# Optimization experiments

Hardware: AMD Instinct MI355X
Metric: run time of the kernel (lower is better)

The kernel has to match this reference:

```python
import jax, jax.numpy as jnp
import numpy as np

# Clebsch-Gordan coefficients in the real basis; l=1 components stored in (y,z,x) order
S2 = 1.0 / np.sqrt(2.0)
S3 = 1.0 / np.sqrt(3.0)
S6 = 1.0 / np.sqrt(6.0)
_C2 = np.zeros((5, 3, 3), np.float32)
_C2[0, 2, 0] = _C2[0, 0, 2] = S2          # ~ xy
_C2[1, 0, 1] = _C2[1, 1, 0] = S2          # ~ yz
_C2[2, 1, 1] = 2.0 * S6                   # ~ 2z^2 - x^2 - y^2
_C2[2, 2, 2] = -S6
_C2[2, 0, 0] = -S6
_C2[3, 2, 1] = _C2[3, 1, 2] = S2          # ~ xz
_C2[4, 2, 2] = S2                          # ~ x^2 - y^2
_C2[4, 0, 0] = -S2
C2 = jnp.asarray(_C2)

N0, N1 = 64, 32        # multiplicities of input 0e / 1o irreps
CUTOFF = 5.0


def basis_functions(pos):
    """pos [N,3] -> (scalars [N,64], l=1 features [N,32,3])."""
    r = jnp.linalg.norm(pos, axis=-1, keepdims=True) + 1e-9        # [N,1]
    d = pos[:, (1, 2, 0)] / r                                       # unit dir, (y,z,x) order
    c0 = jnp.linspace(0.0, CUTOFF, N0, dtype=pos.dtype)
    c1 = jnp.linspace(0.0, CUTOFF, N1, dtype=pos.dtype)
    f0 = jnp.exp(-4.0 * (r - c0) ** 2)                              # [N,64] gaussian RBF
    f1 = jnp.exp(-4.0 * (r - c1) ** 2)                              # [N,32]
    x1 = f1[:, :, None] * d[:, None, :]                             # [N,32,3]
    return f0, x1


def lin_l(x, W):
    # channel mixing within one irrep block; preserves the m axis if present
    if x.ndim == 2:
        return x @ W
    return jnp.einsum('ncm,cd->ndm', x, W)


def tensor_product(a0, a1, b0, b1):
    """Full uvw CG tensor product of (64x0 + 32x1) x (64x0 + 32x1)."""
    N = a0.shape[0]
    # l=0 outputs: 0x0->0 and 1x1->0
    p000 = jnp.einsum('na,nb->nab', a0, b0).reshape(N, -1)                 # [N,4096]
    p110 = jnp.einsum('nam,nbm->nab', a1, b1).reshape(N, -1) * S3          # [N,1024]
    t0 = jnp.concatenate([p000, p110], axis=1)                             # [N,5120]
    # l=1 outputs: 0x1->1, 1x0->1, 1x1->1 (cross product)
    p011 = (a0[:, :, None, None] * b1[:, None, :, :]).reshape(N, -1, 3)    # [N,2048,3]
    p101 = (a1[:, :, None, :] * b0[:, None, :, None]).reshape(N, -1, 3)    # [N,2048,3]
    p111 = (jnp.cross(a1[:, :, None, :], b1[:, None, :, :]) * S2).reshape(N, -1, 3)
    t1 = jnp.concatenate([p011, p101, p111], axis=1)                       # [N,5120,3]
    # l=2 output: 1x1->2 via CG tensor
    t2 = jnp.einsum('nai,nbj,mij->nabm', a1, b1, C2).reshape(N, -1, 5)     # [N,1024,5]
    return t0, t1, t2


def setup_inputs() -> dict:
    key = jax.random.key(0)
    ks = jax.random.split(key, 10)
    N = 4096
    def w(k, i, o):
        return jax.random.normal(k, (i, o), jnp.float32) / np.sqrt(i)
    return {
        'positions': jax.random.normal(ks[0], (N, 3), jnp.float32) * 2.0,
        'W1_0': w(ks[1], 64, 64),
        'W1_1': w(ks[2], 32, 32),
        'W2_0': w(ks[3], 64, 64),
        'W2_1': w(ks[4], 32, 32),
        'W3_0': w(ks[5], 5120, 64),
        'W3_1': w(ks[6], 5120, 32),
        'W3_2': w(ks[7], 1024, 16),
        'W_out': w(ks[8], 240, 7),
        'b_out': jnp.zeros((7,), jnp.float32),
    }


def reference(positions, W1_0, W1_1, W2_0, W2_1, W3_0, W3_1, W3_2, W_out, b_out):
    f0, f1 = basis_functions(positions)                 # 64x0, 32x1
    a0, a1 = lin_l(f0, W1_0), lin_l(f1, W1_1)           # linear1
    b0, b1 = lin_l(f0, W2_0), lin_l(f1, W2_1)           # linear2
    t0, t1, t2 = tensor_product(a0, a1, b0, b1)         # 5120x0, 5120x1, 1024x2
    y0 = lin_l(t0, W3_0)                                # [N,64]
    y1 = lin_l(t1, W3_1)                                # [N,32,3]
    y2 = lin_l(t2, W3_2)                                # [N,16,5]
    N = y0.shape[0]
    feat = jnp.concatenate([y0, y1.reshape(N, -1), y2.reshape(N, -1)], axis=1)  # [N,240]
    return feat @ W_out + b_out                         # [N,7]
```

## Files before the change

### kernel.cpp

```cpp
#include <hip/hip_runtime.h>
#include <math.h>

#define NS2 0.70710678118654752440f
#define NS3 0.57735026918962576451f
#define NS6 0.40824829046386301636f

typedef _Float16 half8 __attribute__((ext_vector_type(8)));

#define OFF_W2   0
#define OFF_GRP  90112
#define GRP_STRIDE 5120

__global__ __launch_bounds__(256) void prep_kernel(
    const float* __restrict__ pos,
    const float* __restrict__ W1_0, const float* __restrict__ W1_1,
    const float* __restrict__ W2_0, const float* __restrict__ W2_1,
    const float* __restrict__ W3_0, const float* __restrict__ W3_1,
    const float* __restrict__ W3_2, const float* __restrict__ Wout,
    const float* __restrict__ bout,
    float* __restrict__ ws, float* __restrict__ out, int N)
{
    __shared__ float smem[2464];
    const int tid = threadIdx.x;

    if (blockIdx.x < 88) {
        float* s_wo = smem;
        for (int i = tid; i < 1680; i += 256) s_wo[i] = Wout[i];
        __syncthreads();
        int R = blockIdx.x * 256 + tid;
        int it = R >> 6, l = R & 63;
        float acc[7] = {0.f,0.f,0.f,0.f,0.f,0.f,0.f};
        if (it < 64) {
            const float* wr = W3_0 + (it*64 + l) * 64;
            #pragma unroll 4
            for (int o = 0; o < 64; o += 4) {
                float4 wv = *(const float4*)(wr + o);
                const float* w0 = s_wo + o * 7;
                #pragma unroll
                for (int k = 0; k < 7; ++k)
                    acc[k] = fmaf(wv.x, w0[k], fmaf(wv.y, w0[7+k],
                             fmaf(wv.z, w0[14+k], fmaf(wv.w, w0[21+k], acc[k]))));
            }
        } else if (it < 160) {
            int s = it - 64, m = s >> 5, a = s & 31;
            const float* wr = W3_1 + (2048 + a*64 + l) * 32;
            #pragma unroll 4
            for (int o = 0; o < 32; o += 4) {
                float4 wv = *(const float4*)(wr + o);
                const float* w0 = s_wo + (64 + o*3 + m) * 7;
                #pragma unroll
                for (int k = 0; k < 7; ++k)
                    acc[k] = fmaf(wv.x, w0[k], fmaf(wv.y, w0[21+k],
                             fmaf(wv.z, w0[42+k], fmaf(wv.w, w0[63+k], acc[k]))));
            }
        } else {
            int it2 = it - 160, ah = l >> 5, bh = l & 31;
            if (it2 < 16) {
                int a = it2*2 + ah;
                const float* wr = W3_0 + (4096 + a*32 + bh) * 64;
                #pragma unroll 4
                for (int o = 0; o < 64; o += 4) {
                    float4 wv = *(const float4*)(wr + o);
                    const float* w0 = s_wo + o * 7;
                    #pragma unroll
                    for (int k = 0; k < 7; ++k)
                        acc[k] = fmaf(wv.x, w0[k], fmaf(wv.y, w0[7+k],
                                 fmaf(wv.z, w0[14+k], fmaf(wv.w, w0[21+k], acc[k]))));
                }
            } else if (it2 < 112) {
                int u2 = it2 - 16, m = u2 >> 5, a = (u2 & 31)*2 + ah;
                const float* wr = W3_1 + (a*32 + bh) * 32;
                #pragma unroll 4
                for (int o = 0; o < 32; o += 4) {
                    float4 wv = *(const float4*)(wr + o);
                    const float* w0 = s_wo + (64 + o*3 + m) * 7;
                    #pragma unroll
                    for (int k = 0; k < 7; ++k)
                        acc[k] = fmaf(wv.x, w0[k], fmaf(wv.y, w0[21+k],
                                 fmaf(wv.z, w0[42+k], fmaf(wv.w, w0[63+k], acc[k]))));
                }
            } else {
                int u2 = it2 - 112, m = u2 >> 4, a = (u2 & 15)*2 + ah;
                const float* wr = W3_2 + (a*32 + bh) * 16;
                #pragma unroll 4
                for (int o = 0; o < 16; o += 4) {
                    float4 wv = *(const float4*)(wr + o);
                    const float* w0 = s_wo + (160 + o*5 + m) * 7;
                    #pragma unroll
                    for (int k = 0; k < 7; ++k)
                        acc[k] = fmaf(wv.x, w0[k], fmaf(wv.y, w0[35+k],
                                 fmaf(wv.z, w0[70+k], fmaf(wv.w, w0[105+k], acc[k]))));
                }
            }
        }
        half8 h;
        #pragma unroll
        for (int k = 0; k < 7; ++k) h[k] = (_Float16)acc[k];
        h[7] = (_Float16)0.f;
        *(half8*)((char*)ws + (size_t)R * 16) = h;
        return;
    }

    float* s_f0   = smem;
    float* s_f1   = smem + 512;
    float* s_a0   = smem + 768;
    float* s_b0   = smem + 1280;
    float* s_A1   = smem + 1792;
    float* s_B1   = smem + 2048;
    float* s_geom = smem + 2304;

    const int g    = blockIdx.x - 88;
    const int base = g * 8;
    float* grp = ws + OFF_GRP + (size_t)g * GRP_STRIDE;
    {
        int d = tid & 63;
        #pragma unroll
        for (int jj = 0; jj < 2; ++jj) {
            int j = (tid >> 6) + jj * 4;
            int n = base + j;
            float px = pos[n*3+0], py = pos[n*3+1], pz = pos[n*3+2];
            float r  = sqrtf(px*px + py*py + pz*pz) + 1e-9f;
            float t0 = r - (5.0f/63.0f) * (float)d;
            s_f0[j*64 + d] = __expf(-4.f * t0 * t0);
        }
        {
            int j = tid >> 5, d1 = tid & 31;
            int n = base + j;
            float px = pos[n*3+0], py = pos[n*3+1], pz = pos[n*3+2];
            float r  = sqrtf(px*px + py*py + pz*pz) + 1e-9f;
            float t1 = r - (5.0f/31.0f) * (float)d1;
            s_f1[j*32 + d1] = __expf(-4.f * t1 * t1);
        }
        if (tid < 8) {
            int n = base + tid;
            float px = pos[n*3+0], py = pos[n*3+1], pz = pos[n*3+2];
            float r  = sqrtf(px*px + py*py + pz*pz) + 1e-9f;
            float iv = 1.0f / r;
            float d0 = py*iv, d1 = pz*iv, d2 = px*iv;
            s_geom[0*8 + tid] = d0;
            s_geom[1*8 + tid] = d1;
            s_geom[2*8 + tid] = d2;
            s_geom[3*8 + tid] = NS3 * (d0*d0 + d1*d1 + d2*d2);
            s_geom[4*8 + tid] = 2.f*NS2*d2*d0;
            s_geom[5*8 + tid] = 2.f*NS2*d0*d1;
            s_geom[6*8 + tid] = NS6*(2.f*d1*d1 - d2*d2 - d0*d0);
            s_geom[7*8 + tid] = 2.f*NS2*d2*d1;
            s_geom[8*8 + tid] = NS2*(d2*d2 - d0*d0);
        }
        if (tid < 56) out[base*7 + tid] = bout[tid % 7];
    }
    __syncthreads();
    {
        int c = tid & 63, jb = tid >> 6;
        float aa0 = 0.f, aa1 = 0.f, ba0 = 0.f, ba1 = 0.f;
        const float* wa = W1_0 + c;
        const float* wb = W2_0 + c;
        #pragma unroll 4
        for (int d = 0; d < 64; ++d) {
            float wav = wa[d*64], wbv = wb[d*64];
            float fA = s_f0[jb*64 + d], fB = s_f0[(jb+4)*64 + d];
            aa0 = fmaf(fA, wav, aa0);  aa1 = fmaf(fB, wav, aa1);
            ba0 = fmaf(fA, wbv, ba0);  ba1 = fmaf(fB, wbv, ba1);
        }
        s_a0[c*8 + jb] = aa0;  s_a0[c*8 + jb + 4] = aa1;
        s_b0[c*8 + jb] = ba0;  s_b0[c*8 + jb + 4] = ba1;

        int c1 = tid & 31, j8 = tid >> 5;
        float aA = 0.f, aB = 0.f;
        const float* wA = W1_1 + c1;
        const float* wB = W2_1 + c1;
        #pragma unroll 4
        for (int d = 0; d < 32; ++d) {
            float f = s_f1[j8*32 + d];
            aA = fmaf(f, wA[d*32], aA);
            aB = fmaf(f, wB[d*32], aB);
        }
        s_A1[c1*8 + j8] = aA;
        s_B1[c1*8 + j8] = aB;
    }
    __syncthreads();
    for (int idx = tid; idx < 5120; idx += 256) {
        float val;
        if (idx < 4352) {
            int r = idx >> 3, j = idx & 7;
            if (r < 64) val = s_a0[r*8 + j];
            else if (r < 160) {
                int s = r - 64;
                val = s_A1[(s & 31)*8 + j] * s_geom[(s >> 5)*8 + j];
            } else {
                int s = r - 160, it2 = s >> 1, half = s & 1;
                if (it2 < 16)        val = s_A1[(it2*2 + half)*8 + j] * s_geom[3*8 + j];
                else if (it2 < 112) { int u2 = it2-16;  val = s_a0[((u2&31)*2 + half)*8 + j] * s_geom[(u2>>5)*8 + j]; }
                else                { int u2 = it2-112; val = s_A1[((u2&15)*2 + half)*8 + j] * s_geom[(4 + (u2>>4))*8 + j]; }
            }
        } else {
            int v = idx - 4352, r = v >> 3, j = v & 7;
            val = (r < 64) ? s_b0[r*8 + j] : s_B1[(r-64)*8 + j];
        }
        grp[idx] = val;
    }
}

__device__ __forceinline__ int it_of(int i, int s) {
    return (i < 20) ? (s*20 + i) : (160 + s*24 + (i - 20));
}

__global__ __launch_bounds__(256) void main_kernel(
    const float* __restrict__ ws, float* __restrict__ out, int N)
{
    __shared__ __align__(16) float s_ug[544*8];
    __shared__ float s_red[4][56];

    const int tid  = threadIdx.x;
    const int w    = tid >> 6;
    const int lane = tid & 63;
    const int bh   = lane & 31, ah = lane >> 5;
    const int g    = blockIdx.x >> 1;
    const int cs   = blockIdx.x & 1;
    const int base = g * 8;
    const int stream = cs*4 + w;
    const float* grp = ws + OFF_GRP + (size_t)g * GRP_STRIDE;
    const half8* wp  = (const half8*)ws;

    half8 ring[4];
    #pragma unroll
    for (int s = 0; s < 4; ++s)
        ring[s] = wp[(size_t)it_of(s, stream)*64 + lane];

    for (int i = tid; i < 1088; i += 256) ((float4*)s_ug)[i] = ((const float4*)grp)[i];
    const float* vb = grp + 4352;
    float4 b0a = *(const float4*)(vb + lane*8);
    float4 b0b = *(const float4*)(vb + lane*8 + 4);
    float4 B1a = *(const float4*)(vb + (64+bh)*8);
    float4 B1b = *(const float4*)(vb + (64+bh)*8 + 4);
    float b0r[8] = {b0a.x,b0a.y,b0a.z,b0a.w,b0b.x,b0b.y,b0b.z,b0b.w};
    float B1r[8] = {B1a.x,B1a.y,B1a.z,B1a.w,B1b.x,B1b.y,B1b.z,B1b.w};
    __syncthreads();

    float acc[8][7];
    #pragma unroll
    for (int j = 0; j < 8; ++j)
        #pragma unroll
        for (int k = 0; k < 7; ++k) acc[j][k] = 0.f;

    const float* ugA = s_ug + stream*20*8;
    #pragma unroll 4
    for (int i = 0; i < 20; ++i) {
        int s = i & 3;
        half8 hv = ring[s];
        ring[s] = wp[(size_t)it_of(i + 4, stream)*64 + lane];
        float gv[7];
        #pragma unroll
        for (int k = 0; k < 7; ++k) gv[k] = (float)hv[k];
        float4 u0 = *(const float4*)(ugA + i*8);
        float4 u1 = *(const float4*)(ugA + i*8 + 4);
        float uv[8] = {u0.x,u0.y,u0.z,u0.w,u1.x,u1.y,u1.z,u1.w};
        #pragma unroll
        for (int j = 0; j < 8; ++j) {
            float p = uv[j] * b0r[j];
            #pragma unroll
            for (int k = 0; k < 7; ++k) acc[j][k] = fmaf(p, gv[k], acc[j][k]);
        }
    }
    const float* ugB = s_ug + (160 + stream*48 + ah)*8;
    #pragma unroll 4
    for (int i = 20; i < 44; ++i) {
        int s = i & 3;
        half8 hv = ring[s];
        int inext = i + 4; if (inext > 43) inext = 43;
        ring[s] = wp[(size_t)it_of(inext, stream)*64 + lane];
        float gv[7];
        #pragma unroll
        for (int k = 0; k < 7; ++k) gv[k] = (float)hv[k];
        float4 u0 = *(const float4*)(ugB + (i-20)*16);
        float4 u1 = *(const float4*)(ugB + (i-20)*16 + 4);
        float uv[8] = {u0.x,u0.y,u0.z,u0.w,u1.x,u1.y,u1.z,u1.w};
        #pragma unroll
        for (int j = 0; j < 8; ++j) {
            float p = uv[j] * B1r[j];
            #pragma unroll
            for (int k = 0; k < 7; ++k) acc[j][k] = fmaf(p, gv[k], acc[j][k]);
        }
    }

    #pragma unroll
    for (int j = 0; j < 8; ++j)
        #pragma unroll
        for (int k = 0; k < 7; ++k) {
            float v = acc[j][k];
            v += __shfl_xor(v, 1, 64);
            v += __shfl_xor(v, 2, 64);
            v += __shfl_xor(v, 4, 64);
            v += __shfl_xor(v, 8, 64);
            v += __shfl_xor(v, 16, 64);
            v += __shfl_xor(v, 32, 64);
            acc[j][k] = v;
        }
    if (lane == 0) {
        #pragma unroll
        for (int j = 0; j < 8; ++j)
            #pragma unroll
            for (int k = 0; k < 7; ++k)
                s_red[w][j*7 + k] = acc[j][k];
    }
    __syncthreads();
    if (tid < 56) {
        float v = s_red[0][tid] + s_red[1][tid] + s_red[2][tid] + s_red[3][tid];
        atomicAdd(&out[base*7 + tid], v);
    }
}

extern "C" void kernel_launch(void* const* d_in, const int* in_sizes, int n_in,
                              void* d_out, int out_size, void* d_ws, size_t ws_size,
                              hipStream_t stream)
{
    const float* pos  = (const float*)d_in[0];
    const float* W1_0 = (const float*)d_in[1];
    const float* W1_1 = (const float*)d_in[2];
    const float* W2_0 = (const float*)d_in[3];
    const float* W2_1 = (const float*)d_in[4];
    const float* W3_0 = (const float*)d_in[5];
    const float* W3_1 = (const float*)d_in[6];
    const float* W3_2 = (const float*)d_in[7];
    const float* Wout = (const float*)d_in[8];
    const float* bout = (const float*)d_in[9];
    float* ws  = (float*)d_ws;
    float* op  = (float*)d_out;
    int N = in_sizes[0] / 3;
    int groups = N / 8;

    prep_kernel<<<88 + groups, 256, 0, stream>>>(pos, W1_0, W1_1, W2_0, W2_1,
                                                 W3_0, W3_1, W3_2, Wout, bout, ws, op, N);
    main_kernel<<<groups * 2, 256, 0, stream>>>(ws, op, N);
}
```

Baseline: 120.0 us.

## Recast main contraction as MFMA f16 GEMM with per-node feature rows

The folded W3·Wout matrix is now stored transposed in f16, padded to 16 output rows. Per-node u/v/geometry features are written as f16 rows, and the main contraction is rebuilt around 16x16x32 f16 MFMA instructions with double-buffered LDS staging of the weight tiles. The grid changes to 64-node groups split eight ways over K, with per-node atomics into the output. This is meant to replace scalar FMA loops and shuffle reductions with matrix-core throughput. The cost is extra f16 rounding of activations and products, hardcoded 512-block grids that assume a fixed N, and padded work on the unused output rows.

```diff
diff --git a/kernel.cpp b/kernel.cpp
--- a/kernel.cpp
+++ b/kernel.cpp
@@ -5,11 +5,14 @@
 #define NS3 0.57735026918962576451f
 #define NS6 0.40824829046386301636f
 
-typedef _Float16 half8 __attribute__((ext_vector_type(8)));
-
-#define OFF_W2   0
-#define OFF_GRP  90112
-#define GRP_STRIDE 5120
+typedef _Float16 f16;
+typedef _Float16 f16x8 __attribute__((ext_vector_type(8)));
+typedef float    f32x4 __attribute__((ext_vector_type(4)));
+
+#define GT_K    22528
+#define UV_ROW  216
+#define OFF_UV  360448
+#define OFF_IDX 1245184
 
 __global__ __launch_bounds__(256) void prep_kernel(
     const float* __restrict__ pos,
@@ -18,7 +21,7 @@
     const float* __restrict__ W3_0, const float* __restrict__ W3_1,
     const float* __restrict__ W3_2, const float* __restrict__ Wout,
     const float* __restrict__ bout,
-    float* __restrict__ ws, float* __restrict__ out, int N)
+    f16* __restrict__ wsh, float* __restrict__ out, int N)
 {
     __shared__ float smem[2464];
     const int tid = threadIdx.x;
@@ -27,91 +30,101 @@
         float* s_wo = smem;
         for (int i = tid; i < 1680; i += 256) s_wo[i] = Wout[i];
         __syncthreads();
-        int R = blockIdx.x * 256 + tid;
-        int it = R >> 6, l = R & 63;
+        int k = blockIdx.x * 256 + tid;
         float acc[7] = {0.f,0.f,0.f,0.f,0.f,0.f,0.f};
-        if (it < 64) {
-            const float* wr = W3_0 + (it*64 + l) * 64;
+        if (k < 4096) {
+            int a = k >> 6, b = k & 63;
+            const float* wr = W3_0 + (a*64 + b) * 64;
             #pragma unroll 4
             for (int o = 0; o < 64; o += 4) {
                 float4 wv = *(const float4*)(wr + o);
                 const float* w0 = s_wo + o * 7;
                 #pragma unroll
-                for (int k = 0; k < 7; ++k)
-                    acc[k] = fmaf(wv.x, w0[k], fmaf(wv.y, w0[7+k],
-                             fmaf(wv.z, w0[14+k], fmaf(wv.w, w0[21+k], acc[k]))));
+                for (int kk = 0; kk < 7; ++kk)
+                    acc[kk] = fmaf(wv.x, w0[kk], fmaf(wv.y, w0[7+kk],
+                              fmaf(wv.z, w0[14+kk], fmaf(wv.w, w0[21+kk], acc[kk]))));
             }
-        } else if (it < 160) {
-            int s = it - 64, m = s >> 5, a = s & 31;
-            const float* wr = W3_1 + (2048 + a*64 + l) * 32;
+        } else if (k < 10240) {
+            int it = k >> 6, s = it - 64, m = s >> 5, a2 = s & 31, l = k & 63;
+            const float* wr = W3_1 + (2048 + a2*64 + l) * 32;
             #pragma unroll 4
             for (int o = 0; o < 32; o += 4) {
                 float4 wv = *(const float4*)(wr + o);
                 const float* w0 = s_wo + (64 + o*3 + m) * 7;
                 #pragma unroll
-                for (int k = 0; k < 7; ++k)
-                    acc[k] = fmaf(wv.x, w0[k], fmaf(wv.y, w0[21+k],
-                             fmaf(wv.z, w0[42+k], fmaf(wv.w, w0[63+k], acc[k]))));
+                for (int kk = 0; kk < 7; ++kk)
+                    acc[kk] = fmaf(wv.x, w0[kk], fmaf(wv.y, w0[21+kk],
+                              fmaf(wv.z, w0[42+kk], fmaf(wv.w, w0[63+kk], acc[kk]))));
             }
         } else {
-            int it2 = it - 160, ah = l >> 5, bh = l & 31;
-            if (it2 < 16) {
-                int a = it2*2 + ah;
-                const float* wr = W3_0 + (4096 + a*32 + bh) * 64;
+            int it2 = (k - 10240) >> 5, l32 = k & 31;
+            if (it2 < 32) {
+                const float* wr = W3_0 + (4096 + it2*32 + l32) * 64;
                 #pragma unroll 4
                 for (int o = 0; o < 64; o += 4) {
                     float4 wv = *(const float4*)(wr + o);
                     const float* w0 = s_wo + o * 7;
                     #pragma unroll
-                    for (int k = 0; k < 7; ++k)
-                        acc[k] = fmaf(wv.x, w0[k], fmaf(wv.y, w0[7+k],
-                                 fmaf(wv.z, w0[14+k], fmaf(wv.w, w0[21+k], acc[k]))));
+                    for (int kk = 0; kk < 7; ++kk)
+                        acc[kk] = fmaf(wv.x, w0[kk], fmaf(wv.y, w0[7+kk],
+                                  fmaf(wv.z, w0[14+kk], fmaf(wv.w, w0[21+kk], acc[kk]))));
                 }
-            } else if (it2 < 112) {
-                int u2 = it2 - 16, m = u2 >> 5, a = (u2 & 31)*2 + ah;
-                const float* wr = W3_1 + (a*32 + bh) * 32;
+            } else if (it2 < 224) {
+                int t = it2 - 32, m = t >> 6, a = t & 63;
+                const float* wr = W3_1 + (a*32 + l32) * 32;
                 #pragma unroll 4
                 for (int o = 0; o < 32; o += 4) {
                     float4 wv = *(const float4*)(wr + o);
                     const float* w0 = s_wo + (64 + o*3 + m) * 7;
                     #pragma unroll
-                    for (int k = 0; k < 7; ++k)
-                        acc[k] = fmaf(wv.x, w0[k], fmaf(wv.y, w0[21+k],
-                                 fmaf(wv.z, w0[42+k], fmaf(wv.w, w0[63+k], acc[k]))));
+                    for (int kk = 0; kk < 7; ++kk)
+                        acc[kk] = fmaf(wv.x, w0[kk], fmaf(wv.y, w0[21+kk],
+                                  fmaf(wv.z, w0[42+kk], fmaf(wv.w, w0[63+kk], acc[kk]))));
                 }
             } else {
-                int u2 = it2 - 112, m = u2 >> 4, a = (u2 & 15)*2 + ah;
-                const float* wr = W3_2 + (a*32 + bh) * 16;
+                int t = it2 - 224, m = t >> 5, a = t & 31;
+                const float* wr = W3_2 + (a*32 + l32) * 16;
                 #pragma unroll 4
                 for (int o = 0; o < 16; o += 4) {
                     float4 wv = *(const float4*)(wr + o);
                     const float* w0 = s_wo + (160 + o*5 + m) * 7;
                     #pragma unroll
-                    for (int k = 0; k < 7; ++k)
-                        acc[k] = fmaf(wv.x, w0[k], fmaf(wv.y, w0[35+k],
-                                 fmaf(wv.z, w0[70+k], fmaf(wv.w, w0[105+k], acc[k]))));
+                    for (int kk = 0; kk < 7; ++kk)
+                        acc[kk] = fmaf(wv.x, w0[kk], fmaf(wv.y, w0[35+kk],
+                                  fmaf(wv.z, w0[70+kk], fmaf(wv.w, w0[105+kk], acc[kk]))));
                 }
             }
         }
-        half8 h;
-        #pragma unroll
-        for (int k = 0; k < 7; ++k) h[k] = (_Float16)acc[k];
-        h[7] = (_Float16)0.f;
-        *(half8*)((char*)ws + (size_t)R * 16) = h;
+        #pragma unroll
+        for (int r = 0; r < 7; ++r)  wsh[(size_t)r * GT_K + k] = (f16)acc[r];
+        #pragma unroll
+        for (int r = 7; r < 16; ++r) wsh[(size_t)r * GT_K + k] = (f16)0.f;
         return;
     }
 
-    float* s_f0   = smem;
-    float* s_f1   = smem + 512;
-    float* s_a0   = smem + 768;
-    float* s_b0   = smem + 1280;
-    float* s_A1   = smem + 1792;
-    float* s_B1   = smem + 2048;
-    float* s_geom = smem + 2304;
-
-    const int g    = blockIdx.x - 88;
-    const int base = g * 8;
-    float* grp = ws + OFF_GRP + (size_t)g * GRP_STRIDE;
+    if (blockIdx.x == 88 + 512) {
+        for (int c = tid; c < 704; c += 256) {
+            int uidx, gidx;
+            if (c < 320) {
+                int it = c >> 1;
+                if (it < 64) { uidx = it; gidx = 9; }
+                else { int s = it - 64; uidx = 64 + (s & 31); gidx = s >> 5; }
+            } else {
+                int it2 = c - 320;
+                if (it2 < 32)       { uidx = 64 + it2;                gidx = 3; }
+                else if (it2 < 224) { int t = it2 - 32;  uidx = t & 63;       gidx = t >> 6; }
+                else                { int t = it2 - 224; uidx = 64 + (t & 31); gidx = 4 + (t >> 5); }
+            }
+            ((unsigned short*)(wsh + OFF_IDX))[c] = (unsigned short)(uidx | (gidx << 8));
+        }
+        return;
+    }
+
+    float* s_f0 = smem;
+    float* s_f1 = smem + 512;
+    const int g8   = blockIdx.x - 88;
+    const int base = g8 * 8;
+    f16* uv = wsh + OFF_UV;
     {
         int d = tid & 63;
         #pragma unroll
@@ -137,15 +150,17 @@
             float r  = sqrtf(px*px + py*py + pz*pz) + 1e-9f;
             float iv = 1.0f / r;
             float d0 = py*iv, d1 = pz*iv, d2 = px*iv;
-            s_geom[0*8 + tid] = d0;
-            s_geom[1*8 + tid] = d1;
-            s_geom[2*8 + tid] = d2;
-            s_geom[3*8 + tid] = NS3 * (d0*d0 + d1*d1 + d2*d2);
-            s_geom[4*8 + tid] = 2.f*NS2*d2*d0;
-            s_geom[5*8 + tid] = 2.f*NS2*d0*d1;
-            s_geom[6*8 + tid] = NS6*(2.f*d1*d1 - d2*d2 - d0*d0);
-            s_geom[7*8 + tid] = 2.f*NS2*d2*d1;
-            s_geom[8*8 + tid] = NS2*(d2*d2 - d0*d0);
+            f16* row = uv + (size_t)n * UV_ROW;
+            row[192+0] = (f16)d0;
+            row[192+1] = (f16)d1;
+            row[192+2] = (f16)d2;
+            row[192+3] = (f16)(NS3 * (d0*d0 + d1*d1 + d2*d2));
+            row[192+4] = (f16)(2.f*NS2*d2*d0);
+            row[192+5] = (f16)(2.f*NS2*d0*d1);
+            row[192+6] = (f16)(NS6*(2.f*d1*d1 - d2*d2 - d0*d0));
+            row[192+7] = (f16)(2.f*NS2*d2*d1);
+            row[192+8] = (f16)(NS2*(d2*d2 - d0*d0));
+            row[201]   = (f16)1.0f;
         }
         if (tid < 56) out[base*7 + tid] = bout[tid % 7];
     }
@@ -162,8 +177,10 @@
             aa0 = fmaf(fA, wav, aa0);  aa1 = fmaf(fB, wav, aa1);
             ba0 = fmaf(fA, wbv, ba0);  ba1 = fmaf(fB, wbv, ba1);
         }
-        s_a0[c*8 + jb] = aa0;  s_a0[c*8 + jb + 4] = aa1;
-        s_b0[c*8 + jb] = ba0;  s_b0[c*8 + jb + 4] = ba1;
+        uv[(size_t)(base+jb  )*UV_ROW +      c] = (f16)aa0;
+        uv[(size_t)(base+jb+4)*UV_ROW +      c] = (f16)aa1;
+        uv[(size_t)(base+jb  )*UV_ROW + 96 + c] = (f16)ba0;
+        uv[(size_t)(base+jb+4)*UV_ROW + 96 + c] = (f16)ba1;
 
         int c1 = tid & 31, j8 = tid >> 5;
         float aA = 0.f, aB = 0.f;
@@ -175,138 +192,92 @@
             aA = fmaf(f, wA[d*32], aA);
             aB = fmaf(f, wB[d*32], aB);
         }
-        s_A1[c1*8 + j8] = aA;
-        s_B1[c1*8 + j8] = aB;
-    }
-    __syncthreads();
-    for (int idx = tid; idx < 5120; idx += 256) {
-        float val;
-        if (idx < 4352) {
-            int r = idx >> 3, j = idx & 7;
-            if (r < 64) val = s_a0[r*8 + j];
-            else if (r < 160) {
-                int s = r - 64;
-                val = s_A1[(s & 31)*8 + j] * s_geom[(s >> 5)*8 + j];
-            } else {
-                int s = r - 160, it2 = s >> 1, half = s & 1;
-                if (it2 < 16)        val = s_A1[(it2*2 + half)*8 + j] * s_geom[3*8 + j];
-                else if (it2 < 112) { int u2 = it2-16;  val = s_a0[((u2&31)*2 + half)*8 + j] * s_geom[(u2>>5)*8 + j]; }
-                else                { int u2 = it2-112; val = s_A1[((u2&15)*2 + half)*8 + j] * s_geom[(4 + (u2>>4))*8 + j]; }
-            }
-        } else {
-            int v = idx - 4352, r = v >> 3, j = v & 7;
-            val = (r < 64) ? s_b0[r*8 + j] : s_B1[(r-64)*8 + j];
-        }
-        grp[idx] = val;
+        uv[(size_t)(base+j8)*UV_ROW +  64 + c1] = (f16)aA;
+        uv[(size_t)(base+j8)*UV_ROW + 160 + c1] = (f16)aB;
     }
 }
 
-__device__ __forceinline__ int it_of(int i, int s) {
-    return (i < 20) ? (s*20 + i) : (160 + s*24 + (i - 20));
-}
-
 __global__ __launch_bounds__(256) void main_kernel(
-    const float* __restrict__ ws, float* __restrict__ out, int N)
+    const f16* __restrict__ wsh, float* __restrict__ out, int N)
 {
-    __shared__ __align__(16) float s_ug[544*8];
-    __shared__ float s_red[4][56];
+    __shared__ f16 s_g[2][16][264];
+    __shared__ f16 s_uv[64][UV_ROW];
+    __shared__ f16 s_ugt[2][64][8];
+    __shared__ unsigned short s_idx[704];
 
     const int tid  = threadIdx.x;
     const int w    = tid >> 6;
     const int lane = tid & 63;
-    const int bh   = lane & 31, ah = lane >> 5;
-    const int g    = blockIdx.x >> 1;
-    const int cs   = blockIdx.x & 1;
-    const int base = g * 8;
-    const int stream = cs*4 + w;
-    const float* grp = ws + OFF_GRP + (size_t)g * GRP_STRIDE;
-    const half8* wp  = (const half8*)ws;
-
-    half8 ring[4];
-    #pragma unroll
-    for (int s = 0; s < 4; ++s)
-        ring[s] = wp[(size_t)it_of(s, stream)*64 + lane];
-
-    for (int i = tid; i < 1088; i += 256) ((float4*)s_ug)[i] = ((const float4*)grp)[i];
-    const float* vb = grp + 4352;
-    float4 b0a = *(const float4*)(vb + lane*8);
-    float4 b0b = *(const float4*)(vb + lane*8 + 4);
-    float4 B1a = *(const float4*)(vb + (64+bh)*8);
-    float4 B1b = *(const float4*)(vb + (64+bh)*8 + 4);
-    float b0r[8] = {b0a.x,b0a.y,b0a.z,b0a.w,b0b.x,b0b.y,b0b.z,b0b.w};
-    float B1r[8] = {B1a.x,B1a.y,B1a.z,B1a.w,B1b.x,B1b.y,B1b.z,B1b.w};
+    const int lq   = lane >> 4;
+    const int lm   = lane & 15;
+    const int g    = blockIdx.x >> 3;
+    const int kq   = blockIdx.x & 7;
+
+    {
+        const uint4* src = (const uint4*)(wsh + OFF_UV + (size_t)g * 64 * UV_ROW);
+        uint4* dst = (uint4*)&s_uv[0][0];
+        for (int j = tid; j < 1728; j += 256) dst[j] = src[j];
+        const unsigned int* isrc = (const unsigned int*)(wsh + OFF_IDX);
+        unsigned int* idst = (unsigned int*)s_idx;
+        for (int j = tid; j < 352; j += 256) idst[j] = isrc[j];
+    }
     __syncthreads();
 
-    float acc[8][7];
-    #pragma unroll
-    for (int j = 0; j < 8; ++j)
-        #pragma unroll
-        for (int k = 0; k < 7; ++k) acc[j][k] = 0.f;
-
-    const float* ugA = s_ug + stream*20*8;
-    #pragma unroll 4
-    for (int i = 0; i < 20; ++i) {
-        int s = i & 3;
-        half8 hv = ring[s];
-        ring[s] = wp[(size_t)it_of(i + 4, stream)*64 + lane];
-        float gv[7];
-        #pragma unroll
-        for (int k = 0; k < 7; ++k) gv[k] = (float)hv[k];
-        float4 u0 = *(const float4*)(ugA + i*8);
-        float4 u1 = *(const float4*)(ugA + i*8 + 4);
-        float uv[8] = {u0.x,u0.y,u0.z,u0.w,u1.x,u1.y,u1.z,u1.w};
-        #pragma unroll
-        for (int j = 0; j < 8; ++j) {
-            float p = uv[j] * b0r[j];
+    const f16* myrow = &s_uv[w*16 + lm][0];
+    f16x8 vA0 = *(const f16x8*)(myrow +  96 + lq*8);
+    f16x8 vA1 = *(const f16x8*)(myrow + 128 + lq*8);
+    f16x8 vB  = *(const f16x8*)(myrow + 160 + lq*8);
+
+    auto c0_of = [&](int t) {
+        return (t < 5) ? (kq*40 + t*8) : (320 + kq*48 + (t-5)*8);
+    };
+    auto stage = [&](int t, int buf) {
+        int c0 = c0_of(t), k0 = c0 * 32;
+        const f16* src = wsh + k0;
+        for (int j = tid; j < 512; j += 256) {
+            int row = j >> 5, col = j & 31;
+            uint4 v = *(const uint4*)(src + (size_t)row * GT_K + col*8);
+            *(uint4*)&s_g[buf][row][col*8] = v;
+        }
+        for (int j = tid; j < 512; j += 256) {
+            int n = j >> 3, s = j & 7;
+            unsigned short ix = s_idx[c0 + s];
+            float u  = (float)s_uv[n][ix & 255];
+            float gg = (float)s_uv[n][192 + (ix >> 8)];
+            s_ugt[buf][n][s] = (f16)(u * gg);
+        }
+    };
+
+    f32x4 acc = {0.f, 0.f, 0.f, 0.f};
+    auto compute = [&](int buf, bool isA) {
+        #pragma unroll
+        for (int s = 0; s < 8; ++s) {
+            f16x8 a = *(const f16x8*)&s_g[buf][lm][s*32 + lq*8];
+            f16 ug  = s_ugt[buf][w*16 + lm][s];
+            f16x8 vv = isA ? ((s & 1) ? vA1 : vA0) : vB;
+            f16x8 b;
             #pragma unroll
-            for (int k = 0; k < 7; ++k) acc[j][k] = fmaf(p, gv[k], acc[j][k]);
-        }
-    }
-    const float* ugB = s_ug + (160 + stream*48 + ah)*8;
-    #pragma unroll 4
-    for (int i = 20; i < 44; ++i) {
-        int s = i & 3;
-        half8 hv = ring[s];
-        int inext = i + 4; if (inext > 43) inext = 43;
-        ring[s] = wp[(size_t)it_of(inext, stream)*64 + lane];
-        float gv[7];
-        #pragma unroll
-        for (int k = 0; k < 7; ++k) gv[k] = (float)hv[k];
-        float4 u0 = *(const float4*)(ugB + (i-20)*16);
-        float4 u1 = *(const float4*)(ugB + (i-20)*16 + 4);
-        float uv[8] = {u0.x,u0.y,u0.z,u0.w,u1.x,u1.y,u1.z,u1.w};
-        #pragma unroll
-        for (int j = 0; j < 8; ++j) {
-            float p = uv[j] * B1r[j];
-            #pragma unroll
-            for (int k = 0; k < 7; ++k) acc[j][k] = fmaf(p, gv[k], acc[j][k]);
-        }
-    }
-
-    #pragma unroll
-    for (int j = 0; j < 8; ++j)
-        #pragma unroll
-        for (int k = 0; k < 7; ++k) {
-            float v = acc[j][k];
-            v += __shfl_xor(v, 1, 64);
-            v += __shfl_xor(v, 2, 64);
-            v += __shfl_xor(v, 4, 64);
-            v += __shfl_xor(v, 8, 64);
-            v += __shfl_xor(v, 16, 64);
-            v += __shfl_xor(v, 32, 64);
-            acc[j][k] = v;
-        }
-    if (lane == 0) {
-        #pragma unroll
-        for (int j = 0; j < 8; ++j)
-            #pragma unroll
-            for (int k = 0; k < 7; ++k)
-                s_red[w][j*7 + k] = acc[j][k];
-    }
+            for (int j2 = 0; j2 < 8; ++j2) b[j2] = vv[j2] * ug;
+            acc = __builtin_amdgcn_mfma_f32_16x16x32_f16(a, b, acc, 0, 0, 0);
+        }
+    };
+
+    stage(0, 0);
     __syncthreads();
-    if (tid < 56) {
-        float v = s_red[0][tid] + s_red[1][tid] + s_red[2][tid] + s_red[3][tid];
-        atomicAdd(&out[base*7 + tid], v);
+    for (int t = 0; t < 11; ++t) {
+        int buf = t & 1;
+        if (t < 10) stage(t + 1, buf ^ 1);
+        compute(buf, t < 5);
+        __syncthreads();
+    }
+
+    int node = g*64 + w*16 + lm;
+    if (lq == 0) {
+        #pragma unroll
+        for (int r = 0; r < 4; ++r) atomicAdd(&out[node*7 + r], acc[r]);
+    } else if (lq == 1) {
+        #pragma unroll
+        for (int r = 0; r < 3; ++r) atomicAdd(&out[node*7 + 4 + r], acc[r]);
     }
 }
 
@@ -324,12 +295,11 @@
     const float* W3_2 = (const float*)d_in[7];
     const float* Wout = (const float*)d_in[8];
     const float* bout = (const float*)d_in[9];
-    float* ws  = (float*)d_ws;
+    f16*   wsh = (f16*)d_ws;
     float* op  = (float*)d_out;
     int N = in_sizes[0] / 3;
-    int groups = N / 8;
-
-    prep_kernel<<<88 + groups, 256, 0, stream>>>(pos, W1_0, W1_1, W2_0, W2_1,
-                                                 W3_0, W3_1, W3_2, Wout, bout, ws, op, N);
-    main_kernel<<<groups * 2, 256, 0, stream>>>(ws, op, N);
+
+    prep_kernel<<<88 + 512 + 1, 256, 0, stream>>>(pos, W1_0, W1_1, W2_0, W2_1,
+                                                  W3_0, W3_1, W3_2, Wout, bout, wsh, op, N);
+    main_kernel<<<512, 256, 0, stream>>>(wsh, op, N);
 }
```

After: 100.7 us. 1.19x faster.
